# Performance work log

Measured on AMD Instinct MI355X. Metric: run time of the kernel, lower is better.

Reference implementation:

```python
import math
import jax, jax.numpy as jnp
import numpy as np

D_HEAD = 64


def setup_inputs() -> dict:
    key = jax.random.key(0)
    ks = jax.random.split(key, 8)
    B, S, D, H, Dh = 2, 2048, 1024, 16, D_HEAD
    return {
        "x": jax.random.normal(ks[0], (B, S, D), dtype=jnp.float32),
        "attention_mask": jnp.ones((B, S), dtype=bool),
        "query_weight": jax.random.normal(ks[1], (H, D, Dh), dtype=jnp.float32),
        "query_bias": jax.random.normal(ks[2], (H, Dh), dtype=jnp.float32),
        "key_weight": jax.random.normal(ks[3], (H, D, Dh), dtype=jnp.float32),
        "key_bias": jax.random.normal(ks[4], (H, Dh), dtype=jnp.float32),
        "value_weight": jax.random.normal(ks[5], (H, D, Dh), dtype=jnp.float32),
        "value_bias": jax.random.normal(ks[6], (H, Dh), dtype=jnp.float32),
        "output_weight": jax.random.normal(ks[7], (D, D), dtype=jnp.float32),
    }


def reference(x, attention_mask, query_weight, query_bias, key_weight, key_bias,
              value_weight, value_bias, output_weight):
    B, S, D = x.shape
    H, _, Dh = query_weight.shape
    # per-head projections: [B, S, H, Dh]
    q = jnp.einsum('bsd,hde->bshe', x, query_weight) + query_bias
    k = jnp.einsum('bsd,hde->bshe', x, key_weight) + key_bias
    v = jnp.einsum('bsd,hde->bshe', x, value_weight) + value_bias
    # scores: [B, H, Sq, Sk]
    scores = jnp.einsum('bqhe,bkhe->bhqk', q, k)
    # additive mask: subtract inf where mask is False (original: score -= where(mask,0,inf))
    neg = jnp.where(attention_mask, 0.0, jnp.inf)[:, None, None, :]
    scores = scores - neg
    probs = jax.nn.softmax(scores / math.sqrt(Dh), axis=3)
    attn = jnp.einsum('bhqk,bkhe->bhqe', probs, v)
    attn = jnp.transpose(attn, (0, 2, 1, 3)).reshape(B, S, H * Dh)
    return jnp.einsum('bsd,de->bse', attn, output_weight)
```

## Files before the change

### kernel.cpp

```cpp
#include <hip/hip_runtime.h>
#include <math.h>

#define BATCH 2
#define SEQ 2048
#define DMODEL 1024
#define NH 16
#define DH 64

typedef short s16x8 __attribute__((ext_vector_type(8)));
typedef float f32x4 __attribute__((ext_vector_type(4)));

__device__ __forceinline__ ushort f2bf(float x) {
    unsigned u = __float_as_uint(x);
    u += 0x7FFFu + ((u >> 16) & 1u);
    return (ushort)(u >> 16);
}
__device__ __forceinline__ float bf2f(ushort h) {
    return __uint_as_float(((unsigned)h) << 16);
}

__global__ __launch_bounds__(256) void transpose_split(
    const float* __restrict__ src, ushort* __restrict__ dhi,
    ushort* __restrict__ dlo, int R, int C, int split)
{
    const size_t zoff = (size_t)blockIdx.z * R * C;
    const int r0 = blockIdx.y * 64, c0 = blockIdx.x * 64;
    __shared__ float T[64][68];
    const int t = threadIdx.x;
    #pragma unroll
    for (int p = 0; p < 4; ++p) {
        const int slot = t + 256 * p;
        const int row = slot >> 4, ch = (slot & 15) * 4;
        *(float4*)&T[row][ch] =
            *(const float4*)&src[zoff + (size_t)(r0 + row) * C + c0 + ch];
    }
    __syncthreads();
    const int e = t >> 2, dch = (t & 3) * 16;
    s16x8 h0, h1, l0, l1;
    #pragma unroll
    for (int j = 0; j < 8; ++j) {
        const float v = T[dch + j][e];
        const ushort hi = f2bf(v);
        h0[j] = (short)hi; l0[j] = (short)f2bf(v - bf2f(hi));
    }
    #pragma unroll
    for (int j = 0; j < 8; ++j) {
        const float v = T[dch + 8 + j][e];
        const ushort hi = f2bf(v);
        h1[j] = (short)hi; l1[j] = (short)f2bf(v - bf2f(hi));
    }
    const size_t ob = zoff + (size_t)(c0 + e) * R + r0 + dch;
    *(s16x8*)&dhi[ob]     = h0;
    *(s16x8*)&dhi[ob + 8] = h1;
    if (split) {
        *(s16x8*)&dlo[ob]     = l0;
        *(s16x8*)&dlo[ob + 8] = l1;
    }
}

__global__ __launch_bounds__(256) void qkv_fused(
    const float* __restrict__ x,
    const ushort* __restrict__ wqThi, const ushort* __restrict__ wqTlo,
    const ushort* __restrict__ wkThi, const ushort* __restrict__ wkTlo,
    const ushort* __restrict__ wvT,
    const float* __restrict__ bq, const float* __restrict__ bk,
    const float* __restrict__ bv,
    ushort* __restrict__ qhi, ushort* __restrict__ qlo,
    ushort* __restrict__ khi, ushort* __restrict__ klo,
    ushort* __restrict__ vT)
{
    const int h = blockIdx.x;
    const int m0 = blockIdx.y * 128;
    const size_t whoff = (size_t)h * DH * DMODEL;

    __shared__ ushort Ah[128 * 64];
    __shared__ ushort Al[128 * 64];
    __shared__ ushort Bqh[64 * 64];
    __shared__ ushort Bql[64 * 64];
    __shared__ ushort Bkh[64 * 64];
    __shared__ ushort Bkl[64 * 64];
    __shared__ ushort Bv [64 * 64];

    const int t = threadIdx.x;
    const int w = t >> 6, g = (t >> 4) & 3, i = t & 15;

    f32x4 aq[2][4] = {}, ak[2][4] = {}, av_[2][4] = {};

    float4 xa[8];
    s16x8 wqh8[2], wql8[2], wkh8[2], wkl8[2], wv8[2];

    #define QKV_LOADX(K0)                                                     \
        _Pragma("unroll")                                                     \
        for (int p = 0; p < 8; ++p) {                                         \
            const int slot = t + 256 * p;                                     \
            const int row = slot >> 4, ch = (slot & 15) * 4;                  \
            xa[p] = *(const float4*)&x[(size_t)(m0 + row) * DMODEL + (K0) + ch]; \
        }
    #define QKV_LOADW(K0)                                                     \
        _Pragma("unroll")                                                     \
        for (int p = 0; p < 2; ++p) {                                         \
            const int slot = t + 256 * p;                                     \
            const size_t off = whoff + (size_t)(slot >> 3) * DMODEL + (K0) + (slot & 7) * 8; \
            wqh8[p] = *(const s16x8*)&wqThi[off];                             \
            wql8[p] = *(const s16x8*)&wqTlo[off];                             \
            wkh8[p] = *(const s16x8*)&wkThi[off];                             \
            wkl8[p] = *(const s16x8*)&wkTlo[off];                             \
            wv8[p]  = *(const s16x8*)&wvT[off];                               \
        }

    QKV_LOADX(0)
    QKV_LOADW(0)

    for (int k0 = 0; k0 < DMODEL; k0 += 64) {
        __syncthreads();

        #pragma unroll
        for (int p = 0; p < 8; ++p) {
            const int slot = t + 256 * p;
            const int row = slot >> 4, ch = (slot & 15) * 4;
            const int cs = ch ^ ((row & 7) * 8);
            const float vv[4] = {xa[p].x, xa[p].y, xa[p].z, xa[p].w};
            ushort4 hh, ll;
            ushort* hp = (ushort*)&hh; ushort* lp = (ushort*)&ll;
            #pragma unroll
            for (int j = 0; j < 4; ++j) {
                const ushort hi = f2bf(vv[j]);
                hp[j] = hi; lp[j] = f2bf(vv[j] - bf2f(hi));
            }
            *(ushort4*)&Ah[row * 64 + cs] = hh;
            *(ushort4*)&Al[row * 64 + cs] = ll;
        }
        #pragma unroll
        for (int p = 0; p < 2; ++p) {
            const int slot = t + 256 * p;
            const int row = slot >> 3;
            const int cs = ((slot & 7) * 8) ^ ((row & 7) * 8);
            *(s16x8*)&Bqh[row * 64 + cs] = wqh8[p];
            *(s16x8*)&Bql[row * 64 + cs] = wql8[p];
            *(s16x8*)&Bkh[row * 64 + cs] = wkh8[p];
            *(s16x8*)&Bkl[row * 64 + cs] = wkl8[p];
            *(s16x8*)&Bv [row * 64 + cs] = wv8[p];
        }

        if (k0 + 64 < DMODEL) {
            QKV_LOADX(k0 + 64)
            QKV_LOADW(k0 + 64)
        }
        __syncthreads();

        #pragma unroll
        for (int sl = 0; sl < 2; ++sl) {
            const int cfr = (sl * 32 + g * 8) ^ ((i & 7) * 8);
            s16x8 ah[2], al[2];
            #pragma unroll
            for (int rf = 0; rf < 2; ++rf) {
                const int ar = w * 32 + rf * 16 + i;
                ah[rf] = *(const s16x8*)&Ah[ar * 64 + cfr];
                al[rf] = *(const s16x8*)&Al[ar * 64 + cfr];
            }
            #pragma unroll
            for (int nb = 0; nb < 4; ++nb) {
                const int br = nb * 16 + i;
                const s16x8 bqh8 = *(const s16x8*)&Bqh[br * 64 + cfr];
                const s16x8 bql8 = *(const s16x8*)&Bql[br * 64 + cfr];
                const s16x8 bkh8 = *(const s16x8*)&Bkh[br * 64 + cfr];
                const s16x8 bkl8 = *(const s16x8*)&Bkl[br * 64 + cfr];
                const s16x8 bv8  = *(const s16x8*)&Bv [br * 64 + cfr];
                #pragma unroll
                for (int rf = 0; rf < 2; ++rf) {
                    aq[rf][nb] = __builtin_amdgcn_mfma_f32_16x16x32_bf16(ah[rf], bqh8, aq[rf][nb], 0, 0, 0);
                    aq[rf][nb] = __builtin_amdgcn_mfma_f32_16x16x32_bf16(al[rf], bqh8, aq[rf][nb], 0, 0, 0);
                    aq[rf][nb] = __builtin_amdgcn_mfma_f32_16x16x32_bf16(ah[rf], bql8, aq[rf][nb], 0, 0, 0);
                    ak[rf][nb] = __builtin_amdgcn_mfma_f32_16x16x32_bf16(ah[rf], bkh8, ak[rf][nb], 0, 0, 0);
                    ak[rf][nb] = __builtin_amdgcn_mfma_f32_16x16x32_bf16(al[rf], bkh8, ak[rf][nb], 0, 0, 0);
                    ak[rf][nb] = __builtin_amdgcn_mfma_f32_16x16x32_bf16(ah[rf], bkl8, ak[rf][nb], 0, 0, 0);
                    av_[rf][nb] = __builtin_amdgcn_mfma_f32_16x16x32_bf16(ah[rf], bv8, av_[rf][nb], 0, 0, 0);
                }
            }
        }
    }
    #undef QKV_LOADX
    #undef QKV_LOADW

    const int b = m0 >> 11;
    const int sloc0 = (m0 & 2047) + w * 32 + g * 4;
    const size_t bh_base = (size_t)(b * NH + h);

    #pragma unroll
    for (int rf = 0; rf < 2; ++rf)
        #pragma unroll
        for (int nb = 0; nb < 4; ++nb) {
            const float bia = bq[h * DH + nb * 16 + i];
            #pragma unroll
            for (int r = 0; r < 4; ++r) {
                const float val = (aq[rf][nb][r] + bia) * 0.125f;
                const ushort hi = f2bf(val);
                const size_t idx = (bh_base * SEQ + sloc0 + rf * 16 + r) * DH + nb * 16 + i;
                qhi[idx] = hi;
                qlo[idx] = f2bf(val - bf2f(hi));
            }
        }
    #pragma unroll
    for (int rf = 0; rf < 2; ++rf)
        #pragma unroll
        for (int nb = 0; nb < 4; ++nb) {
            const float bia = bk[h * DH + nb * 16 + i];
            #pragma unroll
            for (int r = 0; r < 4; ++r) {
                const float val = ak[rf][nb][r] + bia;
                const ushort hi = f2bf(val);
                const size_t idx = (bh_base * SEQ + sloc0 + rf * 16 + r) * DH + nb * 16 + i;
                khi[idx] = hi;
                klo[idx] = f2bf(val - bf2f(hi));
            }
        }
    #pragma unroll
    for (int rf = 0; rf < 2; ++rf)
        #pragma unroll
        for (int nb = 0; nb < 4; ++nb) {
            const float bia = bv[h * DH + nb * 16 + i];
            ushort4 pk; ushort* pp = (ushort*)&pk;
            #pragma unroll
            for (int r = 0; r < 4; ++r)
                pp[r] = f2bf(av_[rf][nb][r] + bia);
            *(ushort4*)&vT[(bh_base * DH + nb * 16 + i) * SEQ + sloc0 + rf * 16] = pk;
        }
}

__global__ __launch_bounds__(256) void flash4(
    const ushort* __restrict__ qhi, const ushort* __restrict__ qlo,
    const ushort* __restrict__ khi, const ushort* __restrict__ klo,
    const ushort* __restrict__ vT, ushort* __restrict__ attn2)
{
    const int bid = blockIdx.x;
    const int id2 = (bid & 7) * 64 + (bid >> 3);
    const int bh = id2 >> 4, qblk = id2 & 15;
    const int bi = bh >> 4, h = bh & 15;
    const int s0 = qblk * 128;

    __shared__ ushort Kh[64 * 72];
    __shared__ ushort Kl[64 * 72];
    __shared__ ushort Vt[64 * 72];

    const int t = threadIdx.x;
    const int w = t >> 6, g = (t >> 4) & 3, i = t & 15;

    s16x8 qh[2][2], ql[2][2];
    #pragma unroll
    for (int grp = 0; grp < 2; ++grp) {
        const size_t qb = ((size_t)bh * SEQ + s0 + w * 32 + grp * 16 + i) * DH;
        #pragma unroll
        for (int sl = 0; sl < 2; ++sl) {
            qh[grp][sl] = *(const s16x8*)&qhi[qb + sl * 32 + g * 8];
            ql[grp][sl] = *(const s16x8*)&qlo[qb + sl * 32 + g * 8];
        }
    }

    int krow[4];
    #pragma unroll
    for (int cb = 0; cb < 4; ++cb) {
        const int gp = i >> 2, r = i & 3;
        const int bb = cb >> 1, hh = cb & 1;
        const int gg = hh ? (gp ^ 2) : gp;
        krow[cb] = 32 * bb + 8 * gg + 4 * hh + r;
    }

    f32x4 acc[2][4] = {};
    float m_i[2] = {-INFINITY, -INFINITY}, l_i[2] = {0.f, 0.f};

    const size_t kbase = (size_t)bh * SEQ * DH;
    const size_t vbase = (size_t)bh * DH * SEQ;

    s16x8 ckh[2], ckl[2], cvt[2];
    #pragma unroll
    for (int p = 0; p < 2; ++p) {
        const int slot = t + 256 * p;
        const int row = slot >> 3, ch = (slot & 7) * 8;
        ckh[p] = *(const s16x8*)&khi[kbase + (size_t)row * DH + ch];
        ckl[p] = *(const s16x8*)&klo[kbase + (size_t)row * DH + ch];
        cvt[p] = *(const s16x8*)&vT[vbase + (size_t)row * SEQ + ch];
    }

    for (int kt = 0; kt < SEQ / 64; ++kt) {
        __syncthreads();
        #pragma unroll
        for (int p = 0; p < 2; ++p) {
            const int slot = t + 256 * p;
            const int row = slot >> 3, ch = (slot & 7) * 8;
            *(s16x8*)&Kh[row * 72 + ch] = ckh[p];
            *(s16x8*)&Kl[row * 72 + ch] = ckl[p];
            *(s16x8*)&Vt[row * 72 + ch] = cvt[p];
        }
        if (kt + 1 < SEQ / 64) {
            #pragma unroll
            for (int p = 0; p < 2; ++p) {
                const int slot = t + 256 * p;
                const int row = slot >> 3, ch = (slot & 7) * 8;
                ckh[p] = *(const s16x8*)&khi[kbase + (size_t)((kt + 1) * 64 + row) * DH + ch];
                ckl[p] = *(const s16x8*)&klo[kbase + (size_t)((kt + 1) * 64 + row) * DH + ch];
                cvt[p] = *(const s16x8*)&vT[vbase + (size_t)row * SEQ + (kt + 1) * 64 + ch];
            }
        }
        __syncthreads();

        f32x4 st[2][4] = {};
        __builtin_amdgcn_s_setprio(1);
        #pragma unroll
        for (int cb = 0; cb < 4; ++cb) {
            #pragma unroll
            for (int sl = 0; sl < 2; ++sl) {
                const int off = krow[cb] * 72 + sl * 32 + g * 8;
                const s16x8 kh = *(const s16x8*)&Kh[off];
                const s16x8 kl = *(const s16x8*)&Kl[off];
                #pragma unroll
                for (int grp = 0; grp < 2; ++grp) {
                    st[grp][cb] = __builtin_amdgcn_mfma_f32_16x16x32_bf16(kh, qh[grp][sl], st[grp][cb], 0, 0, 0);
                    st[grp][cb] = __builtin_amdgcn_mfma_f32_16x16x32_bf16(kh, ql[grp][sl], st[grp][cb], 0, 0, 0);
                    st[grp][cb] = __builtin_amdgcn_mfma_f32_16x16x32_bf16(kl, qh[grp][sl], st[grp][cb], 0, 0, 0);
                }
            }
        }
        __builtin_amdgcn_s_setprio(0);

        s16x8 pa0[2], pa1[2];
        #pragma unroll
        for (int grp = 0; grp < 2; ++grp) {
            float mloc = -INFINITY;
            #pragma unroll
            for (int cb = 0; cb < 4; ++cb)
                #pragma unroll
                for (int r = 0; r < 4; ++r) mloc = fmaxf(mloc, st[grp][cb][r]);
            mloc = fmaxf(mloc, __shfl_xor(mloc, 16));
            mloc = fmaxf(mloc, __shfl_xor(mloc, 32));
            const float m_new = fmaxf(m_i[grp], mloc);
            const float resc = __expf(m_i[grp] - m_new);
            float sum = 0.f;
            #pragma unroll
            for (int cb = 0; cb < 4; ++cb)
                #pragma unroll
                for (int r = 0; r < 4; ++r) {
                    const float pv = __expf(st[grp][cb][r] - m_new);
                    st[grp][cb][r] = pv; sum += pv;
                }
            sum += __shfl_xor(sum, 16);
            sum += __shfl_xor(sum, 32);
            m_i[grp] = m_new;
            l_i[grp] = l_i[grp] * resc + sum;

            unsigned pk[8];
            #pragma unroll
            for (int cb = 0; cb < 4; ++cb) {
                asm volatile("v_cvt_pk_bf16_f32 %0, %1, %2"
                             : "=v"(pk[cb * 2]) : "v"(st[grp][cb][0]), "v"(st[grp][cb][1]));
                asm volatile("v_cvt_pk_bf16_f32 %0, %1, %2"
                             : "=v"(pk[cb * 2 + 1]) : "v"(st[grp][cb][2]), "v"(st[grp][cb][3]));
            }
            asm volatile("v_permlane32_swap_b32 %0, %1" : "+v"(pk[2]), "+v"(pk[3]));
            asm volatile("v_permlane32_swap_b32 %0, %1" : "+v"(pk[3]), "+v"(pk[2]));
            asm volatile("v_permlane32_swap_b32 %0, %1" : "+v"(pk[6]), "+v"(pk[7]));
            asm volatile("v_permlane32_swap_b32 %0, %1" : "+v"(pk[7]), "+v"(pk[6]));
            union { s16x8 v; unsigned u[4]; } a0, a1;
            a0.u[0] = pk[0]; a0.u[1] = pk[1]; a0.u[2] = pk[3]; a0.u[3] = pk[2];
            a1.u[0] = pk[4]; a1.u[1] = pk[5]; a1.u[2] = pk[7]; a1.u[3] = pk[6];
            pa0[grp] = a0.v; pa1[grp] = a1.v;

            #pragma unroll
            for (int r = 0; r < 4; ++r) {
                const float rq = __shfl(resc, g * 4 + r);
                #pragma unroll
                for (int nb = 0; nb < 4; ++nb) acc[grp][nb][r] *= rq;
            }
        }

        __builtin_amdgcn_s_setprio(1);
        #pragma unroll
        for (int b = 0; b < 2; ++b) {
            #pragma unroll
            for (int nb = 0; nb < 4; ++nb) {
                const s16x8 vf = *(const s16x8*)&Vt[(nb * 16 + i) * 72 + b * 32 + g * 8];
                acc[0][nb] = __builtin_amdgcn_mfma_f32_16x16x32_bf16(
                    b ? pa1[0] : pa0[0], vf, acc[0][nb], 0, 0, 0);
                acc[1][nb] = __builtin_amdgcn_mfma_f32_16x16x32_bf16(
                    b ? pa1[1] : pa0[1], vf, acc[1][nb], 0, 0, 0);
            }
        }
        __builtin_amdgcn_s_setprio(0);
    }

    #pragma unroll
    for (int grp = 0; grp < 2; ++grp)
        #pragma unroll
        for (int r = 0; r < 4; ++r) {
            const float lq = __shfl(l_i[grp], g * 4 + r);
            const float inv = 1.0f / lq;
            const int srow = s0 + w * 32 + grp * 16 + g * 4 + r;
            ushort* orow = attn2 + ((size_t)bi * SEQ + srow) * DMODEL + h * DH;
            #pragma unroll
            for (int nb = 0; nb < 4; ++nb)
                orow[nb * 16 + i] = f2bf(acc[grp][nb][r] * inv);
        }
}

__global__ __launch_bounds__(256) void out_mfma(
    const ushort* __restrict__ a, const ushort* __restrict__ woT,
    float* __restrict__ out)
{
    const int n0 = blockIdx.x * 64;
    const int m0 = blockIdx.y * 128;
    __shared__ ushort As[128 * 72];
    __shared__ ushort Bs[64 * 72];
    const int t = threadIdx.x;
    const int w = t >> 6, g = (t >> 4) & 3, i = t & 15;

    f32x4 acc[2][4] = {};
    s16x8 a8[4], b8[2];

    #define OUT_LOAD(K0)                                                      \
        _Pragma("unroll")                                                     \
        for (int p = 0; p < 4; ++p) {                                         \
            const int slot = t + 256 * p;                                     \
            a8[p] = *(const s16x8*)&a[(size_t)(m0 + (slot >> 3)) * DMODEL + (K0) + (slot & 7) * 8]; \
        }                                                                     \
        _Pragma("unroll")                                                     \
        for (int p = 0; p < 2; ++p) {                                         \
            const int slot = t + 256 * p;                                     \
            b8[p] = *(const s16x8*)&woT[(size_t)(n0 + (slot >> 3)) * DMODEL + (K0) + (slot & 7) * 8]; \
        }

    OUT_LOAD(0)

    for (int k0 = 0; k0 < DMODEL; k0 += 64) {
        __syncthreads();
        #pragma unroll
        for (int p = 0; p < 4; ++p) {
            const int slot = t + 256 * p;
            *(s16x8*)&As[(slot >> 3) * 72 + (slot & 7) * 8] = a8[p];
        }
        #pragma unroll
        for (int p = 0; p < 2; ++p) {
            const int slot = t + 256 * p;
            *(s16x8*)&Bs[(slot >> 3) * 72 + (slot & 7) * 8] = b8[p];
        }
        if (k0 + 64 < DMODEL) {
            OUT_LOAD(k0 + 64)
        }
        __syncthreads();

        #pragma unroll
        for (int sl = 0; sl < 2; ++sl) {
            s16x8 af[2];
            #pragma unroll
            for (int rf = 0; rf < 2; ++rf)
                af[rf] = *(const s16x8*)&As[(w * 32 + rf * 16 + i) * 72 + sl * 32 + g * 8];
            #pragma unroll
            for (int nb = 0; nb < 4; ++nb) {
                const s16x8 bf8 = *(const s16x8*)&Bs[(nb * 16 + i) * 72 + sl * 32 + g * 8];
                #pragma unroll
                for (int rf = 0; rf < 2; ++rf)
                    acc[rf][nb] = __builtin_amdgcn_mfma_f32_16x16x32_bf16(af[rf], bf8, acc[rf][nb], 0, 0, 0);
            }
        }
    }
    #undef OUT_LOAD

    #pragma unroll
    for (int rf = 0; rf < 2; ++rf)
        #pragma unroll
        for (int nb = 0; nb < 4; ++nb)
            #pragma unroll
            for (int r = 0; r < 4; ++r)
                out[(size_t)(m0 + w * 32 + rf * 16 + g * 4 + r) * DMODEL + n0 + nb * 16 + i] =
                    acc[rf][nb][r];
}

extern "C" void kernel_launch(void* const* d_in, const int* in_sizes, int n_in,
                              void* d_out, int out_size, void* d_ws, size_t ws_size,
                              hipStream_t stream) {
    const float* x  = (const float*)d_in[0];
    const float* wq = (const float*)d_in[2];
    const float* bq = (const float*)d_in[3];
    const float* wk = (const float*)d_in[4];
    const float* bk = (const float*)d_in[5];
    const float* wv = (const float*)d_in[6];
    const float* bv = (const float*)d_in[7];
    const float* wo = (const float*)d_in[8];
    float* out = (float*)d_out;

    char* ws = (char*)d_ws;
    ushort* wqThi = (ushort*)(ws + 0);
    ushort* wqTlo = (ushort*)(ws + 2097152);
    ushort* wkThi = (ushort*)(ws + 4194304);
    ushort* wkTlo = (ushort*)(ws + 6291456);
    ushort* wvT   = (ushort*)(ws + 8388608);
    ushort* woT   = (ushort*)(ws + 10485760);
    ushort* qhi   = (ushort*)(ws + 12582912);
    ushort* qlo   = (ushort*)(ws + 20971520);
    ushort* khi   = (ushort*)(ws + 29360128);
    ushort* klo   = (ushort*)(ws + 37748736);
    ushort* vTb   = (ushort*)(ws + 46137344);
    ushort* attn2 = (ushort*)(ws + 54525952);

    transpose_split<<<dim3(1, 16, 16), 256, 0, stream>>>(wq, wqThi, wqTlo, DMODEL, DH, 1);
    transpose_split<<<dim3(1, 16, 16), 256, 0, stream>>>(wk, wkThi, wkTlo, DMODEL, DH, 1);
    transpose_split<<<dim3(1, 16, 16), 256, 0, stream>>>(wv, wvT, wvT, DMODEL, DH, 0);
    transpose_split<<<dim3(16, 16, 1), 256, 0, stream>>>(wo, woT, woT, DMODEL, DMODEL, 0);

    qkv_fused<<<dim3(16, 32), 256, 0, stream>>>(x, wqThi, wqTlo, wkThi, wkTlo, wvT,
                                                bq, bk, bv, qhi, qlo, khi, klo, vTb);
    flash4<<<dim3(512), 256, 0, stream>>>(qhi, qlo, khi, klo, vTb, attn2);
    out_mfma<<<dim3(16, 32), 256, 0, stream>>>(attn2, woT, out);
}
```

Measured before the change: 205.7 us.

## Double-buffer QKV GEMM LDS with 32-wide K steps and merge weight transposes

After: 194.4 us. -5.5%, faster.

```diff
diff --git a/kernel.cpp b/kernel.cpp
--- a/kernel.cpp
+++ b/kernel.cpp
@@ -19,12 +19,22 @@
     return __uint_as_float(((unsigned)h) << 16);
 }
 
-__global__ __launch_bounds__(256) void transpose_split(
-    const float* __restrict__ src, ushort* __restrict__ dhi,
-    ushort* __restrict__ dlo, int R, int C, int split)
+__global__ __launch_bounds__(256) void transpose_qkv_w(
+    const float* __restrict__ wq, const float* __restrict__ wk,
+    const float* __restrict__ wv,
+    ushort* __restrict__ qThi, ushort* __restrict__ qTlo,
+    ushort* __restrict__ kThi, ushort* __restrict__ kTlo,
+    ushort* __restrict__ vT)
 {
-    const size_t zoff = (size_t)blockIdx.z * R * C;
-    const int r0 = blockIdx.y * 64, c0 = blockIdx.x * 64;
+    const int z = blockIdx.z;
+    const int which = z >> 4, hh = z & 15;
+    const float* src = (which == 0) ? wq : (which == 1) ? wk : wv;
+    ushort* dhi = (which == 0) ? qThi : (which == 1) ? kThi : vT;
+    ushort* dlo = (which == 0) ? qTlo : (which == 1) ? kTlo : vT;
+    const int split = (which < 2);
+
+    const size_t zoff = (size_t)hh * DMODEL * DH;
+    const int r0 = blockIdx.y * 64;
     __shared__ float T[64][68];
     const int t = threadIdx.x;
     #pragma unroll
@@ -32,7 +42,7 @@
         const int slot = t + 256 * p;
         const int row = slot >> 4, ch = (slot & 15) * 4;
         *(float4*)&T[row][ch] =
-            *(const float4*)&src[zoff + (size_t)(r0 + row) * C + c0 + ch];
+            *(const float4*)&src[zoff + (size_t)(r0 + row) * DH + ch];
     }
     __syncthreads();
     const int e = t >> 2, dch = (t & 3) * 16;
@@ -49,13 +59,38 @@
         const ushort hi = f2bf(v);
         h1[j] = (short)hi; l1[j] = (short)f2bf(v - bf2f(hi));
     }
-    const size_t ob = zoff + (size_t)(c0 + e) * R + r0 + dch;
+    const size_t ob = zoff + (size_t)e * DMODEL + r0 + dch;
     *(s16x8*)&dhi[ob]     = h0;
     *(s16x8*)&dhi[ob + 8] = h1;
     if (split) {
         *(s16x8*)&dlo[ob]     = l0;
         *(s16x8*)&dlo[ob + 8] = l1;
     }
+}
+
+__global__ __launch_bounds__(256) void transpose_wo(
+    const float* __restrict__ src, ushort* __restrict__ dhi)
+{
+    const int r0 = blockIdx.y * 64, c0 = blockIdx.x * 64;
+    __shared__ float T[64][68];
+    const int t = threadIdx.x;
+    #pragma unroll
+    for (int p = 0; p < 4; ++p) {
+        const int slot = t + 256 * p;
+        const int row = slot >> 4, ch = (slot & 15) * 4;
+        *(float4*)&T[row][ch] =
+            *(const float4*)&src[(size_t)(r0 + row) * DMODEL + c0 + ch];
+    }
+    __syncthreads();
+    const int e = t >> 2, dch = (t & 3) * 16;
+    s16x8 h0, h1;
+    #pragma unroll
+    for (int j = 0; j < 8; ++j) h0[j] = (short)f2bf(T[dch + j][e]);
+    #pragma unroll
+    for (int j = 0; j < 8; ++j) h1[j] = (short)f2bf(T[dch + 8 + j][e]);
+    const size_t ob = (size_t)(c0 + e) * DMODEL + r0 + dch;
+    *(s16x8*)&dhi[ob]     = h0;
+    *(s16x8*)&dhi[ob + 8] = h1;
 }
 
 __global__ __launch_bounds__(256) void qkv_fused(
@@ -73,114 +108,101 @@
     const int m0 = blockIdx.y * 128;
     const size_t whoff = (size_t)h * DH * DMODEL;
 
-    __shared__ ushort Ah[128 * 64];
-    __shared__ ushort Al[128 * 64];
-    __shared__ ushort Bqh[64 * 64];
-    __shared__ ushort Bql[64 * 64];
-    __shared__ ushort Bkh[64 * 64];
-    __shared__ ushort Bkl[64 * 64];
-    __shared__ ushort Bv [64 * 64];
+    __shared__ ushort Ah[2][128 * 32];
+    __shared__ ushort Al[2][128 * 32];
+    __shared__ ushort Bqh[2][64 * 32];
+    __shared__ ushort Bql[2][64 * 32];
+    __shared__ ushort Bkh[2][64 * 32];
+    __shared__ ushort Bkl[2][64 * 32];
+    __shared__ ushort Bv [2][64 * 32];
 
     const int t = threadIdx.x;
     const int w = t >> 6, g = (t >> 4) & 3, i = t & 15;
 
     f32x4 aq[2][4] = {}, ak[2][4] = {}, av_[2][4] = {};
 
-    float4 xa[8];
-    s16x8 wqh8[2], wql8[2], wkh8[2], wkl8[2], wv8[2];
-
-    #define QKV_LOADX(K0)                                                     \
+    float4 xa[4];
+    s16x8 wq8h, wq8l, wk8h, wk8l, wv8;
+
+    const int xrow = t >> 3, xch = (t & 7) * 4;
+    const int wrow = t >> 2, wch = (t & 3) * 8;
+    const size_t wbase = whoff + (size_t)wrow * DMODEL + wch;
+
+    #define QKV_LOAD(K0)                                                      \
         _Pragma("unroll")                                                     \
-        for (int p = 0; p < 8; ++p) {                                         \
-            const int slot = t + 256 * p;                                     \
-            const int row = slot >> 4, ch = (slot & 15) * 4;                  \
-            xa[p] = *(const float4*)&x[(size_t)(m0 + row) * DMODEL + (K0) + ch]; \
-        }
-    #define QKV_LOADW(K0)                                                     \
+        for (int p = 0; p < 4; ++p)                                           \
+            xa[p] = *(const float4*)&x[(size_t)(m0 + xrow + 32 * p) * DMODEL + (K0) + xch]; \
+        wq8h = *(const s16x8*)&wqThi[wbase + (K0)];                           \
+        wq8l = *(const s16x8*)&wqTlo[wbase + (K0)];                           \
+        wk8h = *(const s16x8*)&wkThi[wbase + (K0)];                           \
+        wk8l = *(const s16x8*)&wkTlo[wbase + (K0)];                           \
+        wv8  = *(const s16x8*)&wvT[wbase + (K0)];
+
+    #define QKV_STEP(D, K0)                                                   \
+    {                                                                         \
         _Pragma("unroll")                                                     \
-        for (int p = 0; p < 2; ++p) {                                         \
-            const int slot = t + 256 * p;                                     \
-            const size_t off = whoff + (size_t)(slot >> 3) * DMODEL + (K0) + (slot & 7) * 8; \
-            wqh8[p] = *(const s16x8*)&wqThi[off];                             \
-            wql8[p] = *(const s16x8*)&wqTlo[off];                             \
-            wkh8[p] = *(const s16x8*)&wkThi[off];                             \
-            wkl8[p] = *(const s16x8*)&wkTlo[off];                             \
-            wv8[p]  = *(const s16x8*)&wvT[off];                               \
-        }
-
-    QKV_LOADX(0)
-    QKV_LOADW(0)
-
+        for (int p = 0; p < 4; ++p) {                                         \
+            const int row = xrow + 32 * p;                                    \
+            const int cs = xch ^ ((row & 3) * 8);                             \
+            const float vv[4] = {xa[p].x, xa[p].y, xa[p].z, xa[p].w};         \
+            ushort4 hh, ll;                                                   \
+            ushort* hp = (ushort*)&hh; ushort* lp = (ushort*)&ll;             \
+            _Pragma("unroll")                                                 \
+            for (int j = 0; j < 4; ++j) {                                     \
+                const ushort hi = f2bf(vv[j]);                                \
+                hp[j] = hi; lp[j] = f2bf(vv[j] - bf2f(hi));                   \
+            }                                                                 \
+            *(ushort4*)&Ah[D][row * 32 + cs] = hh;                            \
+            *(ushort4*)&Al[D][row * 32 + cs] = ll;                            \
+        }                                                                     \
+        {                                                                     \
+            const int cs = wch ^ ((wrow & 3) * 8);                            \
+            *(s16x8*)&Bqh[D][wrow * 32 + cs] = wq8h;                          \
+            *(s16x8*)&Bql[D][wrow * 32 + cs] = wq8l;                          \
+            *(s16x8*)&Bkh[D][wrow * 32 + cs] = wk8h;                          \
+            *(s16x8*)&Bkl[D][wrow * 32 + cs] = wk8l;                          \
+            *(s16x8*)&Bv [D][wrow * 32 + cs] = wv8;                           \
+        }                                                                     \
+        if ((K0) + 32 < DMODEL) { QKV_LOAD((K0) + 32) }                       \
+        __syncthreads();                                                      \
+        {                                                                     \
+            const int acs = (g * 8) ^ ((i & 3) * 8);                          \
+            s16x8 ah[2], al[2];                                               \
+            _Pragma("unroll")                                                 \
+            for (int rf = 0; rf < 2; ++rf) {                                  \
+                const int ar = w * 32 + rf * 16 + i;                          \
+                ah[rf] = *(const s16x8*)&Ah[D][ar * 32 + acs];                \
+                al[rf] = *(const s16x8*)&Al[D][ar * 32 + acs];                \
+            }                                                                 \
+            _Pragma("unroll")                                                 \
+            for (int nb = 0; nb < 4; ++nb) {                                  \
+                const int br = nb * 16 + i;                                   \
+                const s16x8 bqh8 = *(const s16x8*)&Bqh[D][br * 32 + acs];     \
+                const s16x8 bql8 = *(const s16x8*)&Bql[D][br * 32 + acs];     \
+                const s16x8 bkh8 = *(const s16x8*)&Bkh[D][br * 32 + acs];     \
+                const s16x8 bkl8 = *(const s16x8*)&Bkl[D][br * 32 + acs];     \
+                const s16x8 bv8  = *(const s16x8*)&Bv [D][br * 32 + acs];     \
+                _Pragma("unroll")                                             \
+                for (int rf = 0; rf < 2; ++rf) {                              \
+                    aq[rf][nb] = __builtin_amdgcn_mfma_f32_16x16x32_bf16(ah[rf], bqh8, aq[rf][nb], 0, 0, 0); \
+                    aq[rf][nb] = __builtin_amdgcn_mfma_f32_16x16x32_bf16(al[rf], bqh8, aq[rf][nb], 0, 0, 0); \
+                    aq[rf][nb] = __builtin_amdgcn_mfma_f32_16x16x32_bf16(ah[rf], bql8, aq[rf][nb], 0, 0, 0); \
+                    ak[rf][nb] = __builtin_amdgcn_mfma_f32_16x16x32_bf16(ah[rf], bkh8, ak[rf][nb], 0, 0, 0); \
+                    ak[rf][nb] = __builtin_amdgcn_mfma_f32_16x16x32_bf16(al[rf], bkh8, ak[rf][nb], 0, 0, 0); \
+                    ak[rf][nb] = __builtin_amdgcn_mfma_f32_16x16x32_bf16(ah[rf], bkl8, ak[rf][nb], 0, 0, 0); \
+                    av_[rf][nb] = __builtin_amdgcn_mfma_f32_16x16x32_bf16(ah[rf], bv8, av_[rf][nb], 0, 0, 0); \
+                }                                                             \
+            }                                                                 \
+        }                                                                     \
+    }
+
+    QKV_LOAD(0)
     for (int k0 = 0; k0 < DMODEL; k0 += 64) {
-        __syncthreads();
-
-        #pragma unroll
-        for (int p = 0; p < 8; ++p) {
-            const int slot = t + 256 * p;
-            const int row = slot >> 4, ch = (slot & 15) * 4;
-            const int cs = ch ^ ((row & 7) * 8);
-            const float vv[4] = {xa[p].x, xa[p].y, xa[p].z, xa[p].w};
-            ushort4 hh, ll;
-            ushort* hp = (ushort*)&hh; ushort* lp = (ushort*)&ll;
-            #pragma unroll
-            for (int j = 0; j < 4; ++j) {
-                const ushort hi = f2bf(vv[j]);
-                hp[j] = hi; lp[j] = f2bf(vv[j] - bf2f(hi));
-            }
-            *(ushort4*)&Ah[row * 64 + cs] = hh;
-            *(ushort4*)&Al[row * 64 + cs] = ll;
-        }
-        #pragma unroll
-        for (int p = 0; p < 2; ++p) {
-            const int slot = t + 256 * p;
-            const int row = slot >> 3;
-            const int cs = ((slot & 7) * 8) ^ ((row & 7) * 8);
-            *(s16x8*)&Bqh[row * 64 + cs] = wqh8[p];
-            *(s16x8*)&Bql[row * 64 + cs] = wql8[p];
-            *(s16x8*)&Bkh[row * 64 + cs] = wkh8[p];
-            *(s16x8*)&Bkl[row * 64 + cs] = wkl8[p];
-            *(s16x8*)&Bv [row * 64 + cs] = wv8[p];
-        }
-
-        if (k0 + 64 < DMODEL) {
-            QKV_LOADX(k0 + 64)
-            QKV_LOADW(k0 + 64)
-        }
-        __syncthreads();
-
-        #pragma unroll
-        for (int sl = 0; sl < 2; ++sl) {
-            const int cfr = (sl * 32 + g * 8) ^ ((i & 7) * 8);
-            s16x8 ah[2], al[2];
-            #pragma unroll
-            for (int rf = 0; rf < 2; ++rf) {
-                const int ar = w * 32 + rf * 16 + i;
-                ah[rf] = *(const s16x8*)&Ah[ar * 64 + cfr];
-                al[rf] = *(const s16x8*)&Al[ar * 64 + cfr];
-            }
-            #pragma unroll
-            for (int nb = 0; nb < 4; ++nb) {
-                const int br = nb * 16 + i;
-                const s16x8 bqh8 = *(const s16x8*)&Bqh[br * 64 + cfr];
-                const s16x8 bql8 = *(const s16x8*)&Bql[br * 64 + cfr];
-                const s16x8 bkh8 = *(const s16x8*)&Bkh[br * 64 + cfr];
-                const s16x8 bkl8 = *(const s16x8*)&Bkl[br * 64 + cfr];
-                const s16x8 bv8  = *(const s16x8*)&Bv [br * 64 + cfr];
-                #pragma unroll
-                for (int rf = 0; rf < 2; ++rf) {
-                    aq[rf][nb] = __builtin_amdgcn_mfma_f32_16x16x32_bf16(ah[rf], bqh8, aq[rf][nb], 0, 0, 0);
-                    aq[rf][nb] = __builtin_amdgcn_mfma_f32_16x16x32_bf16(al[rf], bqh8, aq[rf][nb], 0, 0, 0);
-                    aq[rf][nb] = __builtin_amdgcn_mfma_f32_16x16x32_bf16(ah[rf], bql8, aq[rf][nb], 0, 0, 0);
-                    ak[rf][nb] = __builtin_amdgcn_mfma_f32_16x16x32_bf16(ah[rf], bkh8, ak[rf][nb], 0, 0, 0);
-                    ak[rf][nb] = __builtin_amdgcn_mfma_f32_16x16x32_bf16(al[rf], bkh8, ak[rf][nb], 0, 0, 0);
-                    ak[rf][nb] = __builtin_amdgcn_mfma_f32_16x16x32_bf16(ah[rf], bkl8, ak[rf][nb], 0, 0, 0);
-                    av_[rf][nb] = __builtin_amdgcn_mfma_f32_16x16x32_bf16(ah[rf], bv8, av_[rf][nb], 0, 0, 0);
-                }
-            }
-        }
-    }
-    #undef QKV_LOADX
-    #undef QKV_LOADW
+        QKV_STEP(0, k0)
+        QKV_STEP(1, k0 + 32)
+    }
+    #undef QKV_LOAD
+    #undef QKV_STEP
 
     const int b = m0 >> 11;
     const int sloc0 = (m0 & 2047) + w * 32 + g * 4;
@@ -500,10 +522,9 @@
     ushort* vTb   = (ushort*)(ws + 46137344);
     ushort* attn2 = (ushort*)(ws + 54525952);
 
-    transpose_split<<<dim3(1, 16, 16), 256, 0, stream>>>(wq, wqThi, wqTlo, DMODEL, DH, 1);
-    transpose_split<<<dim3(1, 16, 16), 256, 0, stream>>>(wk, wkThi, wkTlo, DMODEL, DH, 1);
-    transpose_split<<<dim3(1, 16, 16), 256, 0, stream>>>(wv, wvT, wvT, DMODEL, DH, 0);
-    transpose_split<<<dim3(16, 16, 1), 256, 0, stream>>>(wo, woT, woT, DMODEL, DMODEL, 0);
+    transpose_qkv_w<<<dim3(1, 16, 48), 256, 0, stream>>>(
+        wq, wk, wv, wqThi, wqTlo, wkThi, wkTlo, wvT);
+    transpose_wo<<<dim3(16, 16), 256, 0, stream>>>(wo, woT);
 
     qkv_fused<<<dim3(16, 32), 256, 0, stream>>>(x, wqThi, wqTlo, wkThi, wkTlo, wvT,
                                                 bq, bk, bv, qhi, qlo, khi, klo, vTb);
```
